# Kernel tuning notes

Hardware: AMD Instinct MI355X
Metric: run time of the kernel (lower is better)

## Reference

```python
import jax, jax.numpy as jnp
import numpy as np

D_MODEL = 1024
N_HEADS = 16
HEAD_DIM = 64
INNER = N_HEADS * HEAD_DIM
D_FF = 4096


def ln_novar(x, w, b):
    # mean-only 'layernorm' (no variance division), per original LayerNormNoVar
    u = jnp.mean(x, axis=-1, keepdims=True)
    return w * (x - u) + b


def setup_inputs() -> dict:
    key = jax.random.key(0)
    ks = jax.random.split(key, 12)
    s = lambda k, shape, scale: jax.random.normal(k, shape, dtype=jnp.float32) * scale
    inp = {
        "src": s(ks[0], (4, 2048, D_MODEL), 1.0),
        "pre_norm_w": jnp.ones((D_MODEL,), jnp.float32),
        "pre_norm_b": jnp.zeros((D_MODEL,), jnp.float32),
        "wq": s(ks[1], (D_MODEL, INNER), 0.02),
        "wk": s(ks[2], (D_MODEL, INNER), 0.02),
        "wv": s(ks[3], (D_MODEL, INNER), 0.02),
        "w_proj": s(ks[4], (INNER, D_MODEL), 0.02),
        "b_proj": jnp.zeros((D_MODEL,), jnp.float32),
        "norm1_w": jnp.ones((D_MODEL,), jnp.float32),
        "norm1_b": jnp.zeros((D_MODEL,), jnp.float32),
        "w1": s(ks[5], (D_MODEL, D_FF), 0.02),
        "b1": jnp.zeros((D_FF,), jnp.float32),
        "w2": s(ks[6], (D_FF, D_MODEL), 0.02),
        "b2": jnp.zeros((D_MODEL,), jnp.float32),
    }
    return inp


def reference(src, pre_norm_w, pre_norm_b, wq, wk, wv, w_proj, b_proj,
              norm1_w, norm1_b, w1, b1, w2, b2):
    B, N, _ = src.shape
    scale = HEAD_DIM ** -0.5
    x = ln_novar(src, pre_norm_w, pre_norm_b)
    q = (x @ wq).reshape(B, N, N_HEADS, HEAD_DIM)
    k = (x @ wk).reshape(B, N, N_HEADS, HEAD_DIM)
    v = (x @ wv).reshape(B, N, N_HEADS, HEAD_DIM)
    attn = jnp.einsum('bqhd,bkhd->bhqk', q, k) * scale
    attn = jax.nn.softmax(attn, axis=-1)
    o = jnp.einsum('bhqk,bkhd->bqhd', attn, v).reshape(B, N, INNER)
    o = o @ w_proj + b_proj
    src = src + o
    src = ln_novar(src, norm1_w, norm1_b)
    ff = jax.nn.relu(src @ w1 + b1) @ w2 + b2
    return src + ff
```

## Files before the change

kernel.cpp:

```cpp
#include <hip/hip_runtime.h>
#include <hip/hip_bf16.h>
#include <stdint.h>

typedef __hip_bfloat16 bf16;
typedef float f32x4 __attribute__((ext_vector_type(4)));
typedef float f32x16 __attribute__((ext_vector_type(16)));
typedef short v8s __attribute__((ext_vector_type(8)));
typedef __bf16 v8bf __attribute__((ext_vector_type(8)));
typedef unsigned int v4u __attribute__((ext_vector_type(4)));
typedef unsigned int u32;

static constexpr int MROWS = 8192;
static constexpr int DM    = 1024;
static constexpr int DFF   = 4096;
static constexpr int SEQ   = 2048;

__device__ __forceinline__ f32x4 mfma16(v8s a, v8s b, f32x4 c) {
  return __builtin_amdgcn_mfma_f32_16x16x32_bf16(
      __builtin_bit_cast(v8bf, a), __builtin_bit_cast(v8bf, b), c, 0, 0, 0);
}
__device__ __forceinline__ f32x16 mfma32(v8s a, v8s b, f32x16 c) {
  return __builtin_amdgcn_mfma_f32_32x32x16_bf16(
      __builtin_bit_cast(v8bf, a), __builtin_bit_cast(v8bf, b), c, 0, 0, 0);
}

__device__ __forceinline__ void gload_lds16(const void* g, void* l) {
  __builtin_amdgcn_global_load_lds(
      (const __attribute__((address_space(1))) void*)g,
      (__attribute__((address_space(3))) void*)l, 16, 0, 0);
}

__device__ __forceinline__ u32 cvtpk_bf16(float a, float b) {
  u32 r;
  asm("v_cvt_pk_bf16_f32 %0, %1, %2" : "=v"(r) : "v"(a), "v"(b));
  return r;
}
__device__ __forceinline__ void pl32swap(u32& x, u32& y) {
  asm volatile("v_permlane32_swap_b32 %0, %1" : "+v"(x), "+v"(y));
}
__device__ __forceinline__ float fast_exp2(float x) {
  float r;
  asm("v_exp_f32 %0, %1" : "=v"(r) : "v"(x));
  return r;
}

__global__ __launch_bounds__(256) void transpose_cast(
    const float* __restrict__ W, bf16* __restrict__ WT, int K, int N) {
  __shared__ float tile[32][33];
  const int c0 = blockIdx.x * 32;
  const int r0 = blockIdx.y * 32;
  const int tx = threadIdx.x & 31, ty = threadIdx.x >> 5;
  #pragma unroll
  for (int i = 0; i < 32; i += 8)
    tile[ty + i][tx] = W[(size_t)(r0 + ty + i) * N + c0 + tx];
  __syncthreads();
  #pragma unroll
  for (int i = 0; i < 32; i += 8)
    WT[(size_t)(c0 + ty + i) * K + r0 + tx] = __float2bfloat16(tile[tx][ty + i]);
}

__global__ __launch_bounds__(256) void ln_novar_kernel(
    const float* __restrict__ x, const float* __restrict__ w,
    const float* __restrict__ b, bf16* __restrict__ ob, float* __restrict__ of) {
  const int row = blockIdx.x;
  const int t = threadIdx.x;
  const float4 v = ((const float4*)(x + (size_t)row * DM))[t];
  float s = v.x + v.y + v.z + v.w;
  #pragma unroll
  for (int off = 32; off > 0; off >>= 1) s += __shfl_down(s, off, 64);
  __shared__ float wsum[4];
  if ((t & 63) == 0) wsum[t >> 6] = s;
  __syncthreads();
  const float u = (wsum[0] + wsum[1] + wsum[2] + wsum[3]) * (1.0f / DM);
  const float4 wv = ((const float4*)w)[t];
  const float4 bv = ((const float4*)b)[t];
  const float o0 = wv.x * (v.x - u) + bv.x;
  const float o1 = wv.y * (v.y - u) + bv.y;
  const float o2 = wv.z * (v.z - u) + bv.z;
  const float o3 = wv.w * (v.w - u) + bv.w;
  bf16* op = ob + (size_t)row * DM + t * 4;
  op[0] = __float2bfloat16(o0); op[1] = __float2bfloat16(o1);
  op[2] = __float2bfloat16(o2); op[3] = __float2bfloat16(o3);
  if (of) {
    float4 o4; o4.x = o0; o4.y = o1; o4.z = o2; o4.w = o3;
    ((float4*)(of + (size_t)row * DM))[t] = o4;
  }
}

#define BM 128
#define BN 256
#define BK 64
#define ASZ (BM * BK)
#define BSZ (BN * BK)
template <int EPI>
__global__ __launch_bounds__(512) void gemm_bt(
    const bf16* __restrict__ A, const bf16* __restrict__ BT,
    bf16* __restrict__ Cb, float* __restrict__ Cf,
    const float* __restrict__ bias, const float* __restrict__ res,
    int M, int Nn, int K) {
  __shared__ __align__(16) bf16 S[3][ASZ + BSZ];

  const int tid = threadIdx.x;
  const int lane = tid & 63;
  const int wave = tid >> 6;
  const int wr = wave >> 2;
  const int wcn = wave & 3;

  const int nwg = gridDim.x;
  const int nbx = Nn / BN;
  int bid = (blockIdx.x & 7) * (nwg >> 3) + (blockIdx.x >> 3);
  const int GM = 4;
  const int grp = bid / (GM * nbx);
  const int rem = bid - grp * (GM * nbx);
  const int by = grp * GM + (rem & (GM - 1));
  const int bx = rem >> 2;
  const int tM = by * BM, tN = bx * BN;

  f32x4 acc[4][4] = {};
  const int nk = K / BK;

  auto STAGE_H = [&](int buf, int kt, int hf) {
    const int k0 = kt * BK;
    bf16* Ab = &S[buf][0];
    bf16* Bb = &S[buf][ASZ];
    {
      const int slot = hf * 512 + tid;
      const int row = slot >> 3, s = slot & 7;
      const int kk = ((s ^ (row & 7)) << 3);
      gload_lds16(A + (size_t)(tM + row) * K + k0 + kk, (void*)(Ab + slot * 8));
    }
    #pragma unroll
    for (int c2 = 0; c2 < 2; ++c2) {
      const int slot = hf * 1024 + c2 * 512 + tid;
      const int row = slot >> 3, s = slot & 7;
      const int kk = ((s ^ (row & 7)) << 3);
      gload_lds16(BT + (size_t)(tN + row) * K + k0 + kk, (void*)(Bb + slot * 8));
    }
  };

  STAGE_H(0, 0, 0); STAGE_H(0, 0, 1);
  STAGE_H(1, 1, 0); STAGE_H(1, 1, 1);
  asm volatile("s_waitcnt vmcnt(6)" ::: "memory");
  __builtin_amdgcn_s_barrier();
  asm volatile("" ::: "memory");

  for (int kt = 0; kt < nk; ++kt) {
    const int cur = kt % 3;
    const bf16* Ab = &S[cur][0];
    const bf16* Bb = &S[cur][ASZ];
    #pragma unroll
    for (int kk = 0; kk < 2; ++kk) {
      const int kslot = kk * 4 + (lane >> 4);
      v8s af[4], bfr[4];
      #pragma unroll
      for (int m = 0; m < 4; ++m) {
        const int row = wr * 64 + m * 16 + (lane & 15);
        af[m] = *(const v8s*)(Ab + (row * 8 + (kslot ^ (row & 7))) * 8);
      }
      #pragma unroll
      for (int n = 0; n < 4; ++n) {
        const int row = wcn * 64 + n * 16 + (lane & 15);
        bfr[n] = *(const v8s*)(Bb + (row * 8 + (kslot ^ (row & 7))) * 8);
      }
      if (kt + 2 < nk) STAGE_H((kt + 2) % 3, kt + 2, kk);
      if (kk == 1) {
        if (kt + 2 < nk) asm volatile("s_waitcnt vmcnt(6)" ::: "memory");
        else             asm volatile("s_waitcnt vmcnt(0)" ::: "memory");
      }
      __builtin_amdgcn_s_barrier();
      asm volatile("" ::: "memory");
      __builtin_amdgcn_s_setprio(1);
      #pragma unroll
      for (int m = 0; m < 4; ++m)
        #pragma unroll
        for (int n = 0; n < 4; ++n)
          acc[m][n] = mfma16(af[m], bfr[n], acc[m][n]);
      __builtin_amdgcn_s_setprio(0);
      asm volatile("" ::: "memory");
      __builtin_amdgcn_s_barrier();
      asm volatile("" ::: "memory");
    }
  }

  #pragma unroll
  for (int m = 0; m < 4; ++m) {
    #pragma unroll
    for (int n = 0; n < 4; ++n) {
      const int row0 = tM + wr * 64 + m * 16 + ((lane >> 4) << 2);
      const int col = tN + wcn * 64 + n * 16 + (lane & 15);
      #pragma unroll
      for (int r = 0; r < 4; ++r) {
        const size_t idx = (size_t)(row0 + r) * Nn + col;
        float v = acc[m][n][r];
        if (EPI == 0) {
          Cb[idx] = __float2bfloat16(v);
        } else if (EPI == 1) {
          v += bias[col];
          v = fmaxf(v, 0.0f);
          Cb[idx] = __float2bfloat16(v);
        } else {
          v += bias[col] + res[idx];
          Cf[idx] = v;
        }
      }
    }
  }
}

__global__ __launch_bounds__(256) void repack_kv(
    const bf16* __restrict__ qkv, bf16* __restrict__ krep,
    bf16* __restrict__ vrep) {
  const int bhkt = blockIdx.x;
  const int bh = bhkt >> 5, kt = bhkt & 31;
  const int b = bh >> 4, h = bh & 15;
  const size_t obase = (size_t)bhkt * 4096;
  #pragma unroll
  for (int it = 0; it < 16; ++it) {
    const int o = it * 256 + threadIdx.x;
    const int ch = o >> 9, rowi = (o >> 3) & 63, e = o & 7;
    krep[obase + o] =
        qkv[(size_t)(b * SEQ + kt * 64 + rowi) * 3072 + 1024 + h * 64 + ch * 8 + e];
    vrep[obase + o] =
        qkv[(size_t)(b * SEQ + kt * 64 + ch * 8 + e) * 3072 + 2048 + h * 64 + rowi];
  }
}

#define PPV(i) ((i) < 16 ? s0[(i) & 15] : s1[(i) & 15])
__global__ __launch_bounds__(256, 4) void attn_kernel(
    const bf16* __restrict__ qkv, const bf16* __restrict__ krep,
    const bf16* __restrict__ vrep, bf16* __restrict__ ob) {
  const int qt = blockIdx.x & 15;
  const int bh = blockIdx.x >> 4;
  const int b = bh >> 4, h = bh & 15;
  const int tid = threadIdx.x;
  const int lane = tid & 63, wave = tid >> 6;
  const int c = lane & 31, hi = lane >> 5;
  const float CEXP = 0.180336880111120426f;

  __shared__ __align__(16) bf16 Ks[2][4096];
  __shared__ __align__(16) bf16 Vs[2][4096];

  const int qrow = qt * 128 + wave * 32 + c;
  const bf16* qp = qkv + (size_t)(b * SEQ + qrow) * 3072 + h * 64;
  v8s qf[4];
  #pragma unroll
  for (int ks = 0; ks < 4; ++ks)
    qf[ks] = *(const v8s*)(qp + ks * 16 + hi * 8);

  f32x16 o0 = {}, o1 = {};
  float mrow = -1e30f, lrow = 0.0f;

  const size_t tilebase = (size_t)(bh * 32) * 4096;
  #pragma unroll
  for (int j = 0; j < 2; ++j) {
    gload_lds16(krep + tilebase + (tid + j * 256) * 8, &Ks[0][(tid + j * 256) * 8]);
    gload_lds16(vrep + tilebase + (tid + j * 256) * 8, &Vs[0][(tid + j * 256) * 8]);
  }
  asm volatile("s_waitcnt vmcnt(0)" ::: "memory");
  __builtin_amdgcn_s_barrier();
  asm volatile("" ::: "memory");

  for (int kt = 0; kt < 32; ++kt) {
    const int cur = kt & 1;
    if (kt < 31) {
      const size_t nb = tilebase + (size_t)(kt + 1) * 4096;
      #pragma unroll
      for (int j = 0; j < 2; ++j) {
        gload_lds16(krep + nb + (tid + j * 256) * 8, &Ks[cur ^ 1][(tid + j * 256) * 8]);
        gload_lds16(vrep + nb + (tid + j * 256) * 8, &Vs[cur ^ 1][(tid + j * 256) * 8]);
      }
    }
    const bf16* KB = Ks[cur];
    const bf16* VB = Vs[cur];

    f32x16 s0 = {}, s1 = {};
    __builtin_amdgcn_s_setprio(1);
    #pragma unroll
    for (int ks = 0; ks < 4; ++ks) {
      const int ch = (2 * ks + hi) * 512;
      v8s a0 = *(const v8s*)(KB + ch + c * 8);
      v8s a1 = *(const v8s*)(KB + ch + (c + 32) * 8);
      s0 = mfma32(a0, qf[ks], s0);
      s1 = mfma32(a1, qf[ks], s1);
    }
    __builtin_amdgcn_s_setprio(0);

    float mA = -1e30f, mB = -1e30f;
    #pragma unroll
    for (int i = 0; i < 16; i += 2) {
      mA = fmaxf(fmaxf(s0[i], s0[i + 1]), mA);
      mB = fmaxf(fmaxf(s1[i], s1[i + 1]), mB);
    }
    float tmax = fmaxf(mA, mB);
    tmax = fmaxf(tmax, __shfl_xor(tmax, 32, 64));
    if (__any(tmax - mrow > 64.0f)) {
      const float mnew = fmaxf(mrow, tmax);
      const float ef = fast_exp2((mrow - mnew) * CEXP);
      mrow = mnew;
      lrow *= ef;
      #pragma unroll
      for (int r = 0; r < 16; ++r) {
        const float efq = __shfl(ef, (r & 3) + 8 * (r >> 2) + 4 * hi, 64);
        o0[r] *= efq;
        o1[r] *= efq;
      }
    }
    const float nmc = -mrow * CEXP;
    float rs0 = 0.0f, rs1 = 0.0f;
    #pragma unroll
    for (int i = 0; i < 16; ++i) {
      s0[i] = fast_exp2(fmaf(s0[i], CEXP, nmc));
      s1[i] = fast_exp2(fmaf(s1[i], CEXP, nmc));
      rs0 += s0[i];
      rs1 += s1[i];
    }
    float rs = rs0 + rs1;
    rs += __shfl_xor(rs, 32, 64);
    lrow += rs;

    v8s pa[4];
    #pragma unroll
    for (int ks = 0; ks < 4; ++ks) {
      u32 x  = cvtpk_bf16(PPV(8 * ks + 0), PPV(8 * ks + 1));
      u32 y  = cvtpk_bf16(PPV(8 * ks + 4), PPV(8 * ks + 5));
      u32 x2 = cvtpk_bf16(PPV(8 * ks + 2), PPV(8 * ks + 3));
      u32 y2 = cvtpk_bf16(PPV(8 * ks + 6), PPV(8 * ks + 7));
      pl32swap(x, y);
      pl32swap(x2, y2);
      v4u w; w.x = x; w.y = x2; w.z = y; w.w = y2;
      pa[ks] = __builtin_bit_cast(v8s, w);
    }

    __builtin_amdgcn_s_setprio(1);
    #pragma unroll
    for (int ks = 0; ks < 4; ++ks) {
      const int ch = (2 * ks + hi) * 512;
      v8s b0 = *(const v8s*)(VB + ch + c * 8);
      v8s b1 = *(const v8s*)(VB + ch + (c + 32) * 8);
      o0 = mfma32(pa[ks], b0, o0);
      o1 = mfma32(pa[ks], b1, o1);
    }
    __builtin_amdgcn_s_setprio(0);

    asm volatile("s_waitcnt vmcnt(0)" ::: "memory");
    __builtin_amdgcn_s_barrier();
    asm volatile("" ::: "memory");
  }

  const float rl = 1.0f / lrow;
  const size_t orow0 = (size_t)(b * SEQ + qt * 128 + wave * 32);
  #pragma unroll
  for (int r = 0; r < 16; ++r) {
    const int q = (r & 3) + 8 * (r >> 2) + 4 * hi;
    const float rq = __shfl(rl, q, 64);
    bf16* op = ob + (orow0 + q) * DM + h * 64;
    op[c] = __float2bfloat16(o0[r] * rq);
    op[32 + c] = __float2bfloat16(o1[r] * rq);
  }
}

extern "C" void kernel_launch(void* const* d_in, const int* in_sizes, int n_in,
                              void* d_out, int out_size, void* d_ws,
                              size_t ws_size, hipStream_t stream) {
  const float* src   = (const float*)d_in[0];
  const float* pnw   = (const float*)d_in[1];
  const float* pnb   = (const float*)d_in[2];
  const float* wq    = (const float*)d_in[3];
  const float* wk    = (const float*)d_in[4];
  const float* wv    = (const float*)d_in[5];
  const float* wproj = (const float*)d_in[6];
  const float* bproj = (const float*)d_in[7];
  const float* n1w   = (const float*)d_in[8];
  const float* n1b   = (const float*)d_in[9];
  const float* w1    = (const float*)d_in[10];
  const float* b1    = (const float*)d_in[11];
  const float* w2    = (const float*)d_in[12];
  const float* b2    = (const float*)d_in[13];
  float* out = (float*)d_out;

  char* ws = (char*)d_ws;
  size_t off = 0;
  bf16* WTqkv = (bf16*)(ws + off); off += (size_t)3072 * 1024 * 2;
  bf16* WTprj = (bf16*)(ws + off); off += (size_t)1024 * 1024 * 2;
  bf16* WT1   = (bf16*)(ws + off); off += (size_t)4096 * 1024 * 2;
  bf16* WT2   = (bf16*)(ws + off); off += (size_t)1024 * 4096 * 2;
  bf16* xb    = (bf16*)(ws + off); off += (size_t)MROWS * DM * 2;
  bf16* qkvb  = (bf16*)(ws + off); off += (size_t)MROWS * 3072 * 2;
  bf16* obuf  = (bf16*)(ws + off); off += (size_t)MROWS * DM * 2;
  float* yf   = (float*)(ws + off); off += (size_t)MROWS * DM * 4;
  bf16* h1    = (bf16*)(ws + off); off += (size_t)MROWS * DFF * 2;
  bf16* krep = h1;
  bf16* vrep = h1 + (size_t)64 * SEQ * 64;

  const dim3 blk(256);
  const dim3 gblk(512);

  transpose_cast<<<dim3(32, 32), blk, 0, stream>>>(wq, WTqkv, 1024, 1024);
  transpose_cast<<<dim3(32, 32), blk, 0, stream>>>(wk, WTqkv + 1024 * 1024, 1024, 1024);
  transpose_cast<<<dim3(32, 32), blk, 0, stream>>>(wv, WTqkv + 2048 * 1024, 1024, 1024);
  transpose_cast<<<dim3(32, 32), blk, 0, stream>>>(wproj, WTprj, 1024, 1024);
  transpose_cast<<<dim3(128, 32), blk, 0, stream>>>(w1, WT1, 1024, 4096);
  transpose_cast<<<dim3(32, 128), blk, 0, stream>>>(w2, WT2, 4096, 1024);

  ln_novar_kernel<<<MROWS, blk, 0, stream>>>(src, pnw, pnb, xb, nullptr);

  gemm_bt<0><<<dim3((3072 / BN) * (MROWS / BM)), gblk, 0, stream>>>(
      xb, WTqkv, qkvb, nullptr, nullptr, nullptr, MROWS, 3072, 1024);

  repack_kv<<<dim3(64 * 32), blk, 0, stream>>>(qkvb, krep, vrep);

  attn_kernel<<<dim3(16 * 64), dim3(256), 0, stream>>>(qkvb, krep, vrep, obuf);

  gemm_bt<2><<<dim3((1024 / BN) * (MROWS / BM)), gblk, 0, stream>>>(
      obuf, WTprj, nullptr, yf, bproj, src, MROWS, 1024, 1024);

  ln_novar_kernel<<<MROWS, blk, 0, stream>>>(yf, n1w, n1b, xb, out);

  gemm_bt<1><<<dim3((4096 / BN) * (MROWS / BM)), gblk, 0, stream>>>(
      xb, WT1, h1, nullptr, b1, nullptr, MROWS, 4096, 1024);

  gemm_bt<2><<<dim3((1024 / BN) * (MROWS / BM)), gblk, 0, stream>>>(
      h1, WT2, nullptr, out, b2, out, MROWS, 1024, 4096);
}
```

Baseline: 432.7 us.

## Software-pipeline GEMM LDS fragment loads and fuse K/V repack into QKV epilogue

The GEMM main loop now issues the whole next tile's global-to-LDS stage at once and double-buffers register fragments, so LDS reads for the next k-half overlap the MFMAs of the current one, with fewer barriers per iteration. A new epilogue variant writes K and V straight into the repacked layouts the attention kernel expects, which removes the separate repack_kv kernel and its extra read of the QKV buffer. Launch bounds now ask for two workgroups per CU, which caps register use. Risks are register pressure from holding two fragment sets and scattered, uncoalesced 2-byte stores in the K/V epilogue.

```diff
diff --git a/kernel.cpp b/kernel.cpp
--- a/kernel.cpp
+++ b/kernel.cpp
@@ -93,7 +93,7 @@
 #define ASZ (BM * BK)
 #define BSZ (BN * BK)
 template <int EPI>
-__global__ __launch_bounds__(512) void gemm_bt(
+__global__ __launch_bounds__(512, 2) void gemm_bt(
     const bf16* __restrict__ A, const bf16* __restrict__ BT,
     bf16* __restrict__ Cb, float* __restrict__ Cf,
     const float* __restrict__ bias, const float* __restrict__ res,
@@ -119,67 +119,81 @@
   f32x4 acc[4][4] = {};
   const int nk = K / BK;
 
-  auto STAGE_H = [&](int buf, int kt, int hf) {
+  auto STAGE = [&](int buf, int kt) {
     const int k0 = kt * BK;
     bf16* Ab = &S[buf][0];
     bf16* Bb = &S[buf][ASZ];
-    {
-      const int slot = hf * 512 + tid;
+    #pragma unroll
+    for (int c = 0; c < 2; ++c) {
+      const int slot = c * 512 + tid;
       const int row = slot >> 3, s = slot & 7;
       const int kk = ((s ^ (row & 7)) << 3);
       gload_lds16(A + (size_t)(tM + row) * K + k0 + kk, (void*)(Ab + slot * 8));
     }
     #pragma unroll
-    for (int c2 = 0; c2 < 2; ++c2) {
-      const int slot = hf * 1024 + c2 * 512 + tid;
+    for (int c = 0; c < 4; ++c) {
+      const int slot = c * 512 + tid;
       const int row = slot >> 3, s = slot & 7;
       const int kk = ((s ^ (row & 7)) << 3);
       gload_lds16(BT + (size_t)(tN + row) * K + k0 + kk, (void*)(Bb + slot * 8));
     }
   };
 
-  STAGE_H(0, 0, 0); STAGE_H(0, 0, 1);
-  STAGE_H(1, 1, 0); STAGE_H(1, 1, 1);
+  auto LD = [&](v8s* af, v8s* bfr, int buf, int kk) {
+    const bf16* Ab = &S[buf][0];
+    const bf16* Bb = &S[buf][ASZ];
+    const int kslot = kk * 4 + (lane >> 4);
+    #pragma unroll
+    for (int m = 0; m < 4; ++m) {
+      const int row = wr * 64 + m * 16 + (lane & 15);
+      af[m] = *(const v8s*)(Ab + (row * 8 + (kslot ^ (row & 7))) * 8);
+    }
+    #pragma unroll
+    for (int n = 0; n < 4; ++n) {
+      const int row = wcn * 64 + n * 16 + (lane & 15);
+      bfr[n] = *(const v8s*)(Bb + (row * 8 + (kslot ^ (row & 7))) * 8);
+    }
+  };
+
+  v8s fA0[4], fB0[4], fA1[4], fB1[4];
+
+  STAGE(0, 0);
+  STAGE(1, 1);
   asm volatile("s_waitcnt vmcnt(6)" ::: "memory");
   __builtin_amdgcn_s_barrier();
   asm volatile("" ::: "memory");
+  LD(fA0, fB0, 0, 0);
 
   for (int kt = 0; kt < nk; ++kt) {
     const int cur = kt % 3;
-    const bf16* Ab = &S[cur][0];
-    const bf16* Bb = &S[cur][ASZ];
-    #pragma unroll
-    for (int kk = 0; kk < 2; ++kk) {
-      const int kslot = kk * 4 + (lane >> 4);
-      v8s af[4], bfr[4];
+    if (kt + 2 < nk) STAGE((kt + 2) % 3, kt + 2);
+
+    LD(fA1, fB1, cur, 1);
+    __builtin_amdgcn_s_setprio(1);
+    #pragma unroll
+    for (int m = 0; m < 4; ++m)
       #pragma unroll
-      for (int m = 0; m < 4; ++m) {
-        const int row = wr * 64 + m * 16 + (lane & 15);
-        af[m] = *(const v8s*)(Ab + (row * 8 + (kslot ^ (row & 7))) * 8);
-      }
+      for (int n = 0; n < 4; ++n)
+        acc[m][n] = mfma16(fA0[m], fB0[n], acc[m][n]);
+    __builtin_amdgcn_s_setprio(0);
+
+    if (kt + 2 < nk) asm volatile("s_waitcnt vmcnt(6)" ::: "memory");
+    else             asm volatile("s_waitcnt vmcnt(0)" ::: "memory");
+    __builtin_amdgcn_s_barrier();
+    asm volatile("" ::: "memory");
+
+    if (kt + 1 < nk) LD(fA0, fB0, (kt + 1) % 3, 0);
+    __builtin_amdgcn_s_setprio(1);
+    #pragma unroll
+    for (int m = 0; m < 4; ++m)
       #pragma unroll
-      for (int n = 0; n < 4; ++n) {
-        const int row = wcn * 64 + n * 16 + (lane & 15);
-        bfr[n] = *(const v8s*)(Bb + (row * 8 + (kslot ^ (row & 7))) * 8);
-      }
-      if (kt + 2 < nk) STAGE_H((kt + 2) % 3, kt + 2, kk);
-      if (kk == 1) {
-        if (kt + 2 < nk) asm volatile("s_waitcnt vmcnt(6)" ::: "memory");
-        else             asm volatile("s_waitcnt vmcnt(0)" ::: "memory");
-      }
-      __builtin_amdgcn_s_barrier();
-      asm volatile("" ::: "memory");
-      __builtin_amdgcn_s_setprio(1);
-      #pragma unroll
-      for (int m = 0; m < 4; ++m)
-        #pragma unroll
-        for (int n = 0; n < 4; ++n)
-          acc[m][n] = mfma16(af[m], bfr[n], acc[m][n]);
-      __builtin_amdgcn_s_setprio(0);
-      asm volatile("" ::: "memory");
-      __builtin_amdgcn_s_barrier();
-      asm volatile("" ::: "memory");
-    }
+      for (int n = 0; n < 4; ++n)
+        acc[m][n] = mfma16(fA1[m], fB1[n], acc[m][n]);
+    __builtin_amdgcn_s_setprio(0);
+
+    asm volatile("" ::: "memory");
+    __builtin_amdgcn_s_barrier();
+    asm volatile("" ::: "memory");
   }
 
   #pragma unroll
@@ -190,38 +204,42 @@
       const int col = tN + wcn * 64 + n * 16 + (lane & 15);
       #pragma unroll
       for (int r = 0; r < 4; ++r) {
-        const size_t idx = (size_t)(row0 + r) * Nn + col;
+        const int row = row0 + r;
         float v = acc[m][n][r];
         if (EPI == 0) {
-          Cb[idx] = __float2bfloat16(v);
+          Cb[(size_t)row * Nn + col] = __float2bfloat16(v);
         } else if (EPI == 1) {
           v += bias[col];
           v = fmaxf(v, 0.0f);
-          Cb[idx] = __float2bfloat16(v);
+          Cb[(size_t)row * Nn + col] = __float2bfloat16(v);
+        } else if (EPI == 2) {
+          v += bias[col] + res[(size_t)row * Nn + col];
+          Cf[(size_t)row * Nn + col] = v;
         } else {
-          v += bias[col] + res[idx];
-          Cf[idx] = v;
+          const int sec = tN >> 10;
+          if (sec == 0) {
+            Cb[(size_t)row * Nn + col] = __float2bfloat16(v);
+          } else {
+            const int b = row >> 11, nn2 = row & 2047;
+            const int ktt = nn2 >> 6, key = nn2 & 63;
+            if (sec == 1) {
+              const int ck = col - 1024;
+              const int h = ck >> 6, dc = (ck >> 3) & 7, e = ck & 7;
+              bf16* krp = (bf16*)(void*)bias;
+              krp[((size_t)((b * 16 + h) * 32 + ktt)) * 4096 + dc * 512 +
+                  key * 8 + e] = __float2bfloat16(v);
+            } else {
+              const int cv = col - 2048;
+              const int h = cv >> 6, d = cv & 63;
+              const int kc = key >> 3, e2 = key & 7;
+              bf16* vrp = (bf16*)(void*)res;
+              vrp[((size_t)((b * 16 + h) * 32 + ktt)) * 4096 + kc * 512 +
+                  d * 8 + e2] = __float2bfloat16(v);
+            }
+          }
         }
       }
     }
-  }
-}
-
-__global__ __launch_bounds__(256) void repack_kv(
-    const bf16* __restrict__ qkv, bf16* __restrict__ krep,
-    bf16* __restrict__ vrep) {
-  const int bhkt = blockIdx.x;
-  const int bh = bhkt >> 5, kt = bhkt & 31;
-  const int b = bh >> 4, h = bh & 15;
-  const size_t obase = (size_t)bhkt * 4096;
-  #pragma unroll
-  for (int it = 0; it < 16; ++it) {
-    const int o = it * 256 + threadIdx.x;
-    const int ch = o >> 9, rowi = (o >> 3) & 63, e = o & 7;
-    krep[obase + o] =
-        qkv[(size_t)(b * SEQ + kt * 64 + rowi) * 3072 + 1024 + h * 64 + ch * 8 + e];
-    vrep[obase + o] =
-        qkv[(size_t)(b * SEQ + kt * 64 + ch * 8 + e) * 3072 + 2048 + h * 64 + rowi];
   }
 }
 
@@ -404,10 +422,9 @@
 
   ln_novar_kernel<<<MROWS, blk, 0, stream>>>(src, pnw, pnb, xb, nullptr);
 
-  gemm_bt<0><<<dim3((3072 / BN) * (MROWS / BM)), gblk, 0, stream>>>(
-      xb, WTqkv, qkvb, nullptr, nullptr, nullptr, MROWS, 3072, 1024);
-
-  repack_kv<<<dim3(64 * 32), blk, 0, stream>>>(qkvb, krep, vrep);
+  gemm_bt<3><<<dim3((3072 / BN) * (MROWS / BM)), gblk, 0, stream>>>(
+      xb, WTqkv, qkvb, nullptr, (const float*)krep, (const float*)vrep,
+      MROWS, 3072, 1024);
 
   attn_kernel<<<dim3(16 * 64), dim3(256), 0, stream>>>(qkvb, krep, vrep, obuf);
 
```

New measurement: 417.6 us. 1.04x faster.
